# Performance work log

Hardware: AMD Instinct MI355X
Metric: run time of the kernel (lower is better)

The kernel has to match this reference:

```python
import jax, jax.numpy as jnp
import numpy as np

EPS = 1e-6
WEIGHT_THRESHOLD = 0.0


def setup_inputs() -> dict:
    key = jax.random.key(0)
    kA, kB, kW = jax.random.split(key, 3)
    bs, n = 200000, 20
    A = jax.random.normal(kA, (bs, n, 3), dtype=jnp.float32)
    B = jax.random.normal(kB, (bs, n, 3), dtype=jnp.float32)
    weights = jax.random.uniform(kW, (bs, n), dtype=jnp.float32)
    return {"A": A, "B": B, "weights": weights}


def reference(A, B, weights):
    """Batched weighted Procrustes (Kabsch). A,B: [bs,n,3], weights: [bs,n].
    Returns SE3 transforms [bs,4,4], matching rigid_transform_3d + integrate_trans."""
    w = jnp.where(weights < WEIGHT_THRESHOLD, 0.0, weights)
    wsum = jnp.sum(w, axis=1, keepdims=True)[:, :, None] + EPS  # [bs,1,1]
    centroid_A = jnp.sum(A * w[:, :, None], axis=1, keepdims=True) / wsum  # [bs,1,3]
    centroid_B = jnp.sum(B * w[:, :, None], axis=1, keepdims=True) / wsum
    Am = A - centroid_A
    Bm = B - centroid_B
    # H = Am^T diag(w) Bm  -> [bs,3,3]
    H = jnp.einsum('bni,bn,bnj->bij', Am, w, Bm)
    U, S, Vh = jnp.linalg.svd(H)          # H = U S Vh
    V = jnp.swapaxes(Vh, -1, -2)          # torch.svd's "Vt" is actually V
    Ut = jnp.swapaxes(U, -1, -2)
    delta = jnp.linalg.det(V @ Ut)        # [bs]
    corr = jnp.broadcast_to(jnp.eye(3, dtype=A.dtype), V.shape).copy()
    corr = corr.at[:, 2, 2].set(delta)
    R = V @ corr @ Ut                     # [bs,3,3]
    t = jnp.swapaxes(centroid_B, 1, 2) - R @ jnp.swapaxes(centroid_A, 1, 2)  # [bs,3,1]
    top = jnp.concatenate([R, t], axis=-1)  # [bs,3,4]
    bottom = jnp.broadcast_to(jnp.array([0.0, 0.0, 0.0, 1.0], dtype=A.dtype), (A.shape[0], 1, 4))
    return jnp.concatenate([top, bottom], axis=1)  # [bs,4,4]
```

## Files before the change

kernel.cpp:

```cpp
#include <hip/hip_runtime.h>

#define EPS_W 1e-6f

__device__ __forceinline__ void solve_from_sums(
    float sw, float Sa0, float Sa1, float Sa2,
    float Sb0, float Sb1, float Sb2,
    float M00, float M01, float M02,
    float M10, float M11, float M12,
    float M20, float M21, float M22,
    float R[9], float t[3])
{
    const float inv = 1.f / (sw + EPS_W);
    const float cA0 = Sa0*inv, cA1 = Sa1*inv, cA2 = Sa2*inv;
    const float cB0 = Sb0*inv, cB1 = Sb1*inv, cB2 = Sb2*inv;

    float H[3][3];
    H[0][0] = M00 - cA0*Sb0 - Sa0*cB0 + sw*cA0*cB0;
    H[0][1] = M01 - cA0*Sb1 - Sa0*cB1 + sw*cA0*cB1;
    H[0][2] = M02 - cA0*Sb2 - Sa0*cB2 + sw*cA0*cB2;
    H[1][0] = M10 - cA1*Sb0 - Sa1*cB0 + sw*cA1*cB0;
    H[1][1] = M11 - cA1*Sb1 - Sa1*cB1 + sw*cA1*cB1;
    H[1][2] = M12 - cA1*Sb2 - Sa1*cB2 + sw*cA1*cB2;
    H[2][0] = M20 - cA2*Sb0 - Sa2*cB0 + sw*cA2*cB0;
    H[2][1] = M21 - cA2*Sb1 - Sa2*cB1 + sw*cA2*cB1;
    H[2][2] = M22 - cA2*Sb2 - Sa2*cB2 + sw*cA2*cB2;

    const float Sxx=H[0][0], Sxy=H[0][1], Sxz=H[0][2];
    const float Syx=H[1][0], Syy=H[1][1], Syz=H[1][2];
    const float Szx=H[2][0], Szy=H[2][1], Szz=H[2][2];

    float Nm[4][4];
    Nm[0][0] =  Sxx+Syy+Szz; Nm[0][1] = Syz-Szy;      Nm[0][2] = Szx-Sxz;      Nm[0][3] = Sxy-Syx;
    Nm[1][0] =  Nm[0][1];    Nm[1][1] = Sxx-Syy-Szz;  Nm[1][2] = Sxy+Syx;      Nm[1][3] = Szx+Sxz;
    Nm[2][0] =  Nm[0][2];    Nm[2][1] = Nm[1][2];     Nm[2][2] = -Sxx+Syy-Szz; Nm[2][3] = Syz+Szy;
    Nm[3][0] =  Nm[0][3];    Nm[3][1] = Nm[1][3];     Nm[3][2] = Nm[2][3];     Nm[3][3] = -Sxx-Syy+Szz;

    float Vv[4][4] = {{1.f,0.f,0.f,0.f},{0.f,1.f,0.f,0.f},{0.f,0.f,1.f,0.f},{0.f,0.f,0.f,1.f}};

    for (int sweep = 0; sweep < 5; ++sweep) {
        #pragma unroll
        for (int pair = 0; pair < 6; ++pair) {
            constexpr int PP[6] = {0,0,0,1,1,2};
            constexpr int QQ[6] = {1,2,3,2,3,3};
            const int p = PP[pair], q = QQ[pair];
            float d  = Nm[p][p] - Nm[q][q];
            float o  = Nm[p][q];
            float r2 = d*d + 4.f*o*o;
            bool tiny = r2 < 1e-30f;
            float rinv = rsqrtf(tiny ? 1.f : r2);
            float hh = 0.5f + 0.5f * fabsf(d) * rinv;
            float ci = rsqrtf(hh);
            float c  = hh * ci;
            float s  = (d < 0.f ? o : -o) * rinv * ci;
            c = tiny ? 1.f : c;
            s = tiny ? 0.f : s;
            #pragma unroll
            for (int k = 0; k < 4; ++k) {
                float akp = Nm[k][p], akq = Nm[k][q];
                Nm[k][p] = c*akp - s*akq;
                Nm[k][q] = s*akp + c*akq;
            }
            #pragma unroll
            for (int k = 0; k < 4; ++k) {
                float apk = Nm[p][k], aqk = Nm[q][k];
                Nm[p][k] = c*apk - s*aqk;
                Nm[q][k] = s*apk + c*aqk;
            }
            #pragma unroll
            for (int k = 0; k < 4; ++k) {
                float vkp = Vv[k][p], vkq = Vv[k][q];
                Vv[k][p] = c*vkp - s*vkq;
                Vv[k][q] = s*vkp + c*vkq;
            }
        }
    }

    float q0=Vv[0][0], q1=Vv[1][0], q2=Vv[2][0], q3=Vv[3][0];
    float best = Nm[0][0];
    #pragma unroll
    for (int m = 1; m < 4; ++m) {
        bool bt = Nm[m][m] > best;
        best = bt ? Nm[m][m] : best;
        q0 = bt ? Vv[0][m] : q0;
        q1 = bt ? Vv[1][m] : q1;
        q2 = bt ? Vv[2][m] : q2;
        q3 = bt ? Vv[3][m] : q3;
    }
    float qn = rsqrtf(q0*q0 + q1*q1 + q2*q2 + q3*q3);
    q0*=qn; q1*=qn; q2*=qn; q3*=qn;

    float R00 = q0*q0+q1*q1-q2*q2-q3*q3;
    float R01 = 2.f*(q1*q2 - q0*q3);
    float R02 = 2.f*(q1*q3 + q0*q2);
    float R10 = 2.f*(q1*q2 + q0*q3);
    float R11 = q0*q0-q1*q1+q2*q2-q3*q3;
    float R12 = 2.f*(q2*q3 - q0*q1);
    float R20 = 2.f*(q1*q3 - q0*q2);
    float R21 = 2.f*(q2*q3 + q0*q1);
    float R22 = q0*q0-q1*q1-q2*q2+q3*q3;

    float trRH  = R00*H[0][0]+R01*H[1][0]+R02*H[2][0]
                + R10*H[0][1]+R11*H[1][1]+R12*H[2][1]
                + R20*H[0][2]+R21*H[1][2]+R22*H[2][2];
    float trRtH = R00*H[0][0]+R01*H[0][1]+R02*H[0][2]
                + R10*H[1][0]+R11*H[1][1]+R12*H[1][2]
                + R20*H[2][0]+R21*H[2][1]+R22*H[2][2];
    if (trRtH > trRH) {
        float tt;
        tt = R01; R01 = R10; R10 = tt;
        tt = R02; R02 = R20; R20 = tt;
        tt = R12; R12 = R21; R21 = tt;
    }

    R[0]=R00; R[1]=R01; R[2]=R02;
    R[3]=R10; R[4]=R11; R[5]=R12;
    R[6]=R20; R[7]=R21; R[8]=R22;
    t[0] = cB0 - (R00*cA0 + R01*cA1 + R02*cA2);
    t[1] = cB1 - (R10*cA0 + R11*cA1 + R12*cA2);
    t[2] = cB2 - (R20*cA0 + R21*cA1 + R22*cA2);
}

__global__ __launch_bounds__(256) void kabsch_pair20_kernel(
    const float* __restrict__ A, const float* __restrict__ B,
    const float* __restrict__ W, float* __restrict__ Out, int bs)
{
    const int tid  = blockIdx.x * blockDim.x + threadIdx.x;
    const int item = tid >> 1;
    const int h    = tid & 1;
    if (item >= bs) return;

    const float2* A2 = reinterpret_cast<const float2*>(A);
    const float2* B2 = reinterpret_cast<const float2*>(B);
    const float2* W2 = reinterpret_cast<const float2*>(W);
    const int abase = item*30 + h*15;
    const int wbase = item*10 + h*5;

    float sw = 0.f;
    float Sa0=0.f,Sa1=0.f,Sa2=0.f, Sb0=0.f,Sb1=0.f,Sb2=0.f;
    float M00=0.f,M01=0.f,M02=0.f,M10=0.f,M11=0.f,M12=0.f,M20=0.f,M21=0.f,M22=0.f;

    #pragma unroll
    for (int g = 0; g < 5; ++g) {
        float2 a0 = A2[abase+3*g+0], a1 = A2[abase+3*g+1], a2 = A2[abase+3*g+2];
        float2 b0 = B2[abase+3*g+0], b1 = B2[abase+3*g+1], b2 = B2[abase+3*g+2];
        float2 wv = W2[wbase+g];
        float w0 = wv.x < 0.f ? 0.f : wv.x;
        float w1 = wv.y < 0.f ? 0.f : wv.y;

        {
            float ax=a0.x, ay=a0.y, az=a1.x;
            float bx=b0.x, by=b0.y, bz=b1.x;
            sw += w0;
            float wax=w0*ax, way=w0*ay, waz=w0*az;
            Sa0+=wax; Sa1+=way; Sa2+=waz;
            Sb0+=w0*bx; Sb1+=w0*by; Sb2+=w0*bz;
            M00+=wax*bx; M01+=wax*by; M02+=wax*bz;
            M10+=way*bx; M11+=way*by; M12+=way*bz;
            M20+=waz*bx; M21+=waz*by; M22+=waz*bz;
        }
        {
            float ax=a1.y, ay=a2.x, az=a2.y;
            float bx=b1.y, by=b2.x, bz=b2.y;
            sw += w1;
            float wax=w1*ax, way=w1*ay, waz=w1*az;
            Sa0+=wax; Sa1+=way; Sa2+=waz;
            Sb0+=w1*bx; Sb1+=w1*by; Sb2+=w1*bz;
            M00+=wax*bx; M01+=wax*by; M02+=wax*bz;
            M10+=way*bx; M11+=way*by; M12+=way*bz;
            M20+=waz*bx; M21+=waz*by; M22+=waz*bz;
        }
    }

    sw  += __shfl_xor(sw, 1);
    Sa0 += __shfl_xor(Sa0,1); Sa1 += __shfl_xor(Sa1,1); Sa2 += __shfl_xor(Sa2,1);
    Sb0 += __shfl_xor(Sb0,1); Sb1 += __shfl_xor(Sb1,1); Sb2 += __shfl_xor(Sb2,1);
    M00 += __shfl_xor(M00,1); M01 += __shfl_xor(M01,1); M02 += __shfl_xor(M02,1);
    M10 += __shfl_xor(M10,1); M11 += __shfl_xor(M11,1); M12 += __shfl_xor(M12,1);
    M20 += __shfl_xor(M20,1); M21 += __shfl_xor(M21,1); M22 += __shfl_xor(M22,1);

    float R[9], t[3];
    solve_from_sums(sw,Sa0,Sa1,Sa2,Sb0,Sb1,Sb2,
                    M00,M01,M02,M10,M11,M12,M20,M21,M22, R, t);

    float4 va = h ? make_float4(R[6],R[7],R[8],t[2]) : make_float4(R[0],R[1],R[2],t[0]);
    float4 vb = h ? make_float4(0.f,0.f,0.f,1.f)     : make_float4(R[3],R[4],R[5],t[1]);
    float4* O4 = reinterpret_cast<float4*>(Out + (size_t)item * 16);
    O4[2*h]   = va;
    O4[2*h+1] = vb;
}

__global__ __launch_bounds__(256) void kabsch_generic_kernel(
    const float* __restrict__ A, const float* __restrict__ B,
    const float* __restrict__ W, float* __restrict__ Out,
    int bs, int n)
{
    const int b = blockIdx.x * blockDim.x + threadIdx.x;
    if (b >= bs) return;

    float sw = 0.f;
    float Sa0=0.f,Sa1=0.f,Sa2=0.f, Sb0=0.f,Sb1=0.f,Sb2=0.f;
    float M00=0.f,M01=0.f,M02=0.f,M10=0.f,M11=0.f,M12=0.f,M20=0.f,M21=0.f,M22=0.f;

    for (int j = 0; j < n; ++j) {
        const float* ap = A + ((size_t)b * n + j) * 3;
        const float* bp = B + ((size_t)b * n + j) * 3;
        float w = W[(size_t)b * n + j];
        w = w < 0.f ? 0.f : w;
        float ax=ap[0], ay=ap[1], az=ap[2];
        float bx=bp[0], by=bp[1], bz=bp[2];
        sw += w;
        float wax = w*ax, way = w*ay, waz = w*az;
        Sa0 += wax; Sa1 += way; Sa2 += waz;
        Sb0 += w*bx; Sb1 += w*by; Sb2 += w*bz;
        M00 += wax*bx; M01 += wax*by; M02 += wax*bz;
        M10 += way*bx; M11 += way*by; M12 += way*bz;
        M20 += waz*bx; M21 += waz*by; M22 += waz*bz;
    }

    float R[9], t[3];
    solve_from_sums(sw,Sa0,Sa1,Sa2,Sb0,Sb1,Sb2,
                    M00,M01,M02,M10,M11,M12,M20,M21,M22, R, t);

    float4* O4 = reinterpret_cast<float4*>(Out + (size_t)b * 16);
    O4[0] = make_float4(R[0], R[1], R[2], t[0]);
    O4[1] = make_float4(R[3], R[4], R[5], t[1]);
    O4[2] = make_float4(R[6], R[7], R[8], t[2]);
    O4[3] = make_float4(0.f, 0.f, 0.f, 1.f);
}

extern "C" void kernel_launch(void* const* d_in, const int* in_sizes, int n_in,
                              void* d_out, int out_size, void* d_ws, size_t ws_size,
                              hipStream_t stream) {
    const float* A = (const float*)d_in[0];
    const float* B = (const float*)d_in[1];
    const float* W = (const float*)d_in[2];
    float* Out = (float*)d_out;
    const int bs = out_size / 16;
    const int n  = (bs > 0) ? (in_sizes[2] / bs) : 0;
    const int threads = 256;
    if (n == 20) {
        const int total = bs * 2;
        const int blocks = (total + threads - 1) / threads;
        hipLaunchKernelGGL(kabsch_pair20_kernel, dim3(blocks), dim3(threads), 0, stream,
                           A, B, W, Out, bs);
    } else {
        const int blocks = (bs + threads - 1) / threads;
        hipLaunchKernelGGL(kabsch_generic_kernel, dim3(blocks), dim3(threads), 0, stream,
                           A, B, W, Out, bs, n);
    }
}
```

Before: 157.1 us.

## Compact per-item solve into one thread via shared memory and use fast rsq/rcp

```diff
diff --git a/kernel.cpp b/kernel.cpp
--- a/kernel.cpp
+++ b/kernel.cpp
@@ -2,28 +2,29 @@
 
 #define EPS_W 1e-6f
 
-__device__ __forceinline__ void solve_from_sums(
-    float sw, float Sa0, float Sa1, float Sa2,
-    float Sb0, float Sb1, float Sb2,
-    float M00, float M01, float M02,
-    float M10, float M11, float M12,
-    float M20, float M21, float M22,
-    float R[9], float t[3])
+__device__ __forceinline__ float fast_rsq(float x) { return __builtin_amdgcn_rsqf(x); }
+__device__ __forceinline__ float fast_rcp(float x) { return __builtin_amdgcn_rcpf(x); }
+
+__device__ __forceinline__ void solve16(const float S[16], float R[9], float t[3])
 {
-    const float inv = 1.f / (sw + EPS_W);
+    const float sw  = S[0];
+    const float Sa0 = S[1], Sa1 = S[2], Sa2 = S[3];
+    const float Sb0 = S[4], Sb1 = S[5], Sb2 = S[6];
+
+    const float inv = fast_rcp(sw + EPS_W);
     const float cA0 = Sa0*inv, cA1 = Sa1*inv, cA2 = Sa2*inv;
     const float cB0 = Sb0*inv, cB1 = Sb1*inv, cB2 = Sb2*inv;
 
     float H[3][3];
-    H[0][0] = M00 - cA0*Sb0 - Sa0*cB0 + sw*cA0*cB0;
-    H[0][1] = M01 - cA0*Sb1 - Sa0*cB1 + sw*cA0*cB1;
-    H[0][2] = M02 - cA0*Sb2 - Sa0*cB2 + sw*cA0*cB2;
-    H[1][0] = M10 - cA1*Sb0 - Sa1*cB0 + sw*cA1*cB0;
-    H[1][1] = M11 - cA1*Sb1 - Sa1*cB1 + sw*cA1*cB1;
-    H[1][2] = M12 - cA1*Sb2 - Sa1*cB2 + sw*cA1*cB2;
-    H[2][0] = M20 - cA2*Sb0 - Sa2*cB0 + sw*cA2*cB0;
-    H[2][1] = M21 - cA2*Sb1 - Sa2*cB1 + sw*cA2*cB1;
-    H[2][2] = M22 - cA2*Sb2 - Sa2*cB2 + sw*cA2*cB2;
+    H[0][0] = S[7]  - cA0*Sb0 - Sa0*cB0 + sw*cA0*cB0;
+    H[0][1] = S[8]  - cA0*Sb1 - Sa0*cB1 + sw*cA0*cB1;
+    H[0][2] = S[9]  - cA0*Sb2 - Sa0*cB2 + sw*cA0*cB2;
+    H[1][0] = S[10] - cA1*Sb0 - Sa1*cB0 + sw*cA1*cB0;
+    H[1][1] = S[11] - cA1*Sb1 - Sa1*cB1 + sw*cA1*cB1;
+    H[1][2] = S[12] - cA1*Sb2 - Sa1*cB2 + sw*cA1*cB2;
+    H[2][0] = S[13] - cA2*Sb0 - Sa2*cB0 + sw*cA2*cB0;
+    H[2][1] = S[14] - cA2*Sb1 - Sa2*cB1 + sw*cA2*cB1;
+    H[2][2] = S[15] - cA2*Sb2 - Sa2*cB2 + sw*cA2*cB2;
 
     const float Sxx=H[0][0], Sxy=H[0][1], Sxz=H[0][2];
     const float Syx=H[1][0], Syy=H[1][1], Syz=H[1][2];
@@ -47,9 +48,9 @@
             float o  = Nm[p][q];
             float r2 = d*d + 4.f*o*o;
             bool tiny = r2 < 1e-30f;
-            float rinv = rsqrtf(tiny ? 1.f : r2);
+            float rinv = fast_rsq(tiny ? 1.f : r2);
             float hh = 0.5f + 0.5f * fabsf(d) * rinv;
-            float ci = rsqrtf(hh);
+            float ci = fast_rsq(hh);
             float c  = hh * ci;
             float s  = (d < 0.f ? o : -o) * rinv * ci;
             c = tiny ? 1.f : c;
@@ -86,7 +87,7 @@
         q2 = bt ? Vv[2][m] : q2;
         q3 = bt ? Vv[3][m] : q3;
     }
-    float qn = rsqrtf(q0*q0 + q1*q1 + q2*q2 + q3*q3);
+    float qn = fast_rsq(q0*q0 + q1*q1 + q2*q2 + q3*q3);
     q0*=qn; q1*=qn; q2*=qn; q3*=qn;
 
     float R00 = q0*q0+q1*q1-q2*q2-q3*q3;
@@ -99,12 +100,12 @@
     float R21 = 2.f*(q2*q3 + q0*q1);
     float R22 = q0*q0-q1*q1-q2*q2+q3*q3;
 
-    float trRH  = R00*H[0][0]+R01*H[1][0]+R02*H[2][0]
-                + R10*H[0][1]+R11*H[1][1]+R12*H[2][1]
-                + R20*H[0][2]+R21*H[1][2]+R22*H[2][2];
-    float trRtH = R00*H[0][0]+R01*H[0][1]+R02*H[0][2]
-                + R10*H[1][0]+R11*H[1][1]+R12*H[1][2]
-                + R20*H[2][0]+R21*H[2][1]+R22*H[2][2];
+    float trRH  = R00*Sxx+R01*Syx+R02*Szx
+                + R10*Sxy+R11*Syy+R12*Szy
+                + R20*Sxz+R21*Syz+R22*Szz;
+    float trRtH = R00*Sxx+R01*Sxy+R02*Sxz
+                + R10*Syx+R11*Syy+R12*Syz
+                + R20*Szx+R21*Szy+R22*Szz;
     if (trRtH > trRH) {
         float tt;
         tt = R01; R01 = R10; R10 = tt;
@@ -120,20 +121,24 @@
     t[2] = cB2 - (R20*cA0 + R21*cA1 + R22*cA2);
 }
 
-__global__ __launch_bounds__(256) void kabsch_pair20_kernel(
+__global__ __launch_bounds__(256) void kabsch_fused20_kernel(
     const float* __restrict__ A, const float* __restrict__ B,
     const float* __restrict__ W, float* __restrict__ Out, int bs)
 {
-    const int tid  = blockIdx.x * blockDim.x + threadIdx.x;
-    const int item = tid >> 1;
-    const int h    = tid & 1;
-    if (item >= bs) return;
+    __shared__ float sums[128][17];
+
+    const int tid = threadIdx.x;
+    const int blk = blockIdx.x;
+    const int il  = tid >> 1;
+    const int h   = tid & 1;
+    int item = blk * 128 + il;
+    int itemc = item < bs ? item : (bs - 1);
 
     const float2* A2 = reinterpret_cast<const float2*>(A);
     const float2* B2 = reinterpret_cast<const float2*>(B);
     const float2* W2 = reinterpret_cast<const float2*>(W);
-    const int abase = item*30 + h*15;
-    const int wbase = item*10 + h*5;
+    const int abase = itemc*30 + h*15;
+    const int wbase = itemc*10 + h*5;
 
     float sw = 0.f;
     float Sa0=0.f,Sa1=0.f,Sa2=0.f, Sb0=0.f,Sb1=0.f,Sb2=0.f;
@@ -178,15 +183,31 @@
     M10 += __shfl_xor(M10,1); M11 += __shfl_xor(M11,1); M12 += __shfl_xor(M12,1);
     M20 += __shfl_xor(M20,1); M21 += __shfl_xor(M21,1); M22 += __shfl_xor(M22,1);
 
-    float R[9], t[3];
-    solve_from_sums(sw,Sa0,Sa1,Sa2,Sb0,Sb1,Sb2,
-                    M00,M01,M02,M10,M11,M12,M20,M21,M22, R, t);
-
-    float4 va = h ? make_float4(R[6],R[7],R[8],t[2]) : make_float4(R[0],R[1],R[2],t[0]);
-    float4 vb = h ? make_float4(0.f,0.f,0.f,1.f)     : make_float4(R[3],R[4],R[5],t[1]);
-    float4* O4 = reinterpret_cast<float4*>(Out + (size_t)item * 16);
-    O4[2*h]   = va;
-    O4[2*h+1] = vb;
+    if (h == 0) {
+        sums[il][0]=sw;
+        sums[il][1]=Sa0;  sums[il][2]=Sa1;  sums[il][3]=Sa2;
+        sums[il][4]=Sb0;  sums[il][5]=Sb1;  sums[il][6]=Sb2;
+        sums[il][7]=M00;  sums[il][8]=M01;  sums[il][9]=M02;
+        sums[il][10]=M10; sums[il][11]=M11; sums[il][12]=M12;
+        sums[il][13]=M20; sums[il][14]=M21; sums[il][15]=M22;
+    }
+    __syncthreads();
+
+    if (tid < 128) {
+        const int item2 = blk * 128 + tid;
+        if (item2 < bs) {
+            float S[16];
+            #pragma unroll
+            for (int k = 0; k < 16; ++k) S[k] = sums[tid][k];
+            float R[9], t[3];
+            solve16(S, R, t);
+            float4* O4 = reinterpret_cast<float4*>(Out + (size_t)item2 * 16);
+            O4[0] = make_float4(R[0], R[1], R[2], t[0]);
+            O4[1] = make_float4(R[3], R[4], R[5], t[1]);
+            O4[2] = make_float4(R[6], R[7], R[8], t[2]);
+            O4[3] = make_float4(0.f, 0.f, 0.f, 1.f);
+        }
+    }
 }
 
 __global__ __launch_bounds__(256) void kabsch_generic_kernel(
@@ -197,9 +218,9 @@
     const int b = blockIdx.x * blockDim.x + threadIdx.x;
     if (b >= bs) return;
 
-    float sw = 0.f;
-    float Sa0=0.f,Sa1=0.f,Sa2=0.f, Sb0=0.f,Sb1=0.f,Sb2=0.f;
-    float M00=0.f,M01=0.f,M02=0.f,M10=0.f,M11=0.f,M12=0.f,M20=0.f,M21=0.f,M22=0.f;
+    float S[16];
+    #pragma unroll
+    for (int k = 0; k < 16; ++k) S[k] = 0.f;
 
     for (int j = 0; j < n; ++j) {
         const float* ap = A + ((size_t)b * n + j) * 3;
@@ -208,18 +229,17 @@
         w = w < 0.f ? 0.f : w;
         float ax=ap[0], ay=ap[1], az=ap[2];
         float bx=bp[0], by=bp[1], bz=bp[2];
-        sw += w;
+        S[0] += w;
         float wax = w*ax, way = w*ay, waz = w*az;
-        Sa0 += wax; Sa1 += way; Sa2 += waz;
-        Sb0 += w*bx; Sb1 += w*by; Sb2 += w*bz;
-        M00 += wax*bx; M01 += wax*by; M02 += wax*bz;
-        M10 += way*bx; M11 += way*by; M12 += way*bz;
-        M20 += waz*bx; M21 += waz*by; M22 += waz*bz;
+        S[1] += wax; S[2] += way; S[3] += waz;
+        S[4] += w*bx; S[5] += w*by; S[6] += w*bz;
+        S[7] += wax*bx; S[8]  += wax*by; S[9]  += wax*bz;
+        S[10]+= way*bx; S[11] += way*by; S[12] += way*bz;
+        S[13]+= waz*bx; S[14] += waz*by; S[15] += waz*bz;
     }
 
     float R[9], t[3];
-    solve_from_sums(sw,Sa0,Sa1,Sa2,Sb0,Sb1,Sb2,
-                    M00,M01,M02,M10,M11,M12,M20,M21,M22, R, t);
+    solve16(S, R, t);
 
     float4* O4 = reinterpret_cast<float4*>(Out + (size_t)b * 16);
     O4[0] = make_float4(R[0], R[1], R[2], t[0]);
@@ -237,15 +257,13 @@
     float* Out = (float*)d_out;
     const int bs = out_size / 16;
     const int n  = (bs > 0) ? (in_sizes[2] / bs) : 0;
-    const int threads = 256;
     if (n == 20) {
-        const int total = bs * 2;
-        const int blocks = (total + threads - 1) / threads;
-        hipLaunchKernelGGL(kabsch_pair20_kernel, dim3(blocks), dim3(threads), 0, stream,
+        const int blocks = (bs + 127) / 128;
+        hipLaunchKernelGGL(kabsch_fused20_kernel, dim3(blocks), dim3(256), 0, stream,
                            A, B, W, Out, bs);
     } else {
-        const int blocks = (bs + threads - 1) / threads;
-        hipLaunchKernelGGL(kabsch_generic_kernel, dim3(blocks), dim3(threads), 0, stream,
+        const int blocks = (bs + 255) / 256;
+        hipLaunchKernelGGL(kabsch_generic_kernel, dim3(blocks), dim3(256), 0, stream,
                            A, B, W, Out, bs, n);
     }
 }
```

New measurement: 146.4 us. 6.8% less time.
